# Performance work log

Measured on AMD Instinct MI355X. Metric: run time of the kernel, lower is better.

## Reference

```python
import jax, jax.numpy as jnp
import numpy as np

EPS = 1e-4

def setup_inputs() -> dict:
    key = jax.random.key(0)
    x = jax.random.normal(key, (16, 256, 8192), dtype=jnp.float32)
    return {"x": x}

def reference(x):
    # x: [B, C, T]; cumulative (causal) normalization along time axis
    T = x.shape[-1]
    count = jnp.arange(1, T + 1, dtype=x.dtype).reshape(1, 1, T)
    cum_sum = jnp.cumsum(x, axis=-1)
    cum_pow_sum = jnp.cumsum(x * x, axis=-1)
    cum_mean = cum_sum / count
    cum_var = cum_pow_sum / count - cum_mean * cum_mean
    cum_std = jnp.sqrt(cum_var + EPS)
    return (x - cum_mean) / cum_std
```

## Files before the change

### kernel.cpp

```cpp
#include <hip/hip_runtime.h>
#include <math.h>

#define ROW_T   8192
#define THREADS 256
#define ITEMS   32
#define EPSV    1e-4f

__device__ __forceinline__ int pad_idx(int i) { return i + (i >> 5); }

__global__ __launch_bounds__(THREADS, 4)
void cumnorm_kernel(const float* __restrict__ x, float* __restrict__ out) {
    __shared__ float lds[ROW_T + ROW_T / 32];
    __shared__ float wsum[4];
    __shared__ float wssum[4];

    const int t = threadIdx.x;
    const long long rowbase = (long long)blockIdx.x * ROW_T;
    const float* __restrict__ xr = x + rowbase;
    float* __restrict__ outr = out + rowbase;

    #pragma unroll
    for (int j = 0; j < 8; ++j) {
        const int fi = (j * THREADS + t) * 4;
        const float4 v = *reinterpret_cast<const float4*>(xr + fi);
        lds[pad_idx(fi + 0)] = v.x;
        lds[pad_idx(fi + 1)] = v.y;
        lds[pad_idx(fi + 2)] = v.z;
        lds[pad_idx(fi + 3)] = v.w;
    }
    __syncthreads();

    float xv[ITEMS];
    float s = 0.f, ss = 0.f;
    const int cbase = t * 33;
    #pragma unroll
    for (int j = 0; j < ITEMS; ++j) {
        const float v = lds[cbase + j];
        xv[j] = v;
        s += v;
        ss += v * v;
    }

    const int lane = t & 63;
    const int wid  = t >> 6;
    float is = s, iss = ss;
    #pragma unroll
    for (int off = 1; off < 64; off <<= 1) {
        const float us  = __shfl_up(is, off);
        const float uss = __shfl_up(iss, off);
        if (lane >= off) { is += us; iss += uss; }
    }
    if (lane == 63) { wsum[wid] = is; wssum[wid] = iss; }
    __syncthreads();

    float carry_s = 0.f, carry_ss = 0.f;
    #pragma unroll
    for (int w = 0; w < 4; ++w) {
        if (w < wid) { carry_s += wsum[w]; carry_ss += wssum[w]; }
    }
    float S  = carry_s  + (is  - s);
    float SS = carry_ss + (iss - ss);

    const int ebase = t * ITEMS;
    #pragma unroll
    for (int j = 0; j < ITEMS; ++j) {
        const float v = xv[j];
        S  += v;
        SS += v * v;
        const float inv  = 1.0f / (float)(ebase + j + 1);
        const float mean = S * inv;
        const float var  = fmaf(SS, inv, -(mean * mean));
        lds[cbase + j] = (v - mean) * rsqrtf(var + EPSV);
    }
    __syncthreads();

    #pragma unroll
    for (int j = 0; j < 8; ++j) {
        const int fi = (j * THREADS + t) * 4;
        float4 v;
        v.x = lds[pad_idx(fi + 0)];
        v.y = lds[pad_idx(fi + 1)];
        v.z = lds[pad_idx(fi + 2)];
        v.w = lds[pad_idx(fi + 3)];
        *reinterpret_cast<float4*>(outr + fi) = v;
    }
}

extern "C" void kernel_launch(void* const* d_in, const int* in_sizes, int n_in,
                              void* d_out, int out_size, void* d_ws, size_t ws_size,
                              hipStream_t stream) {
    const float* x = (const float*)d_in[0];
    float* out = (float*)d_out;
    const int rows = out_size / ROW_T;
    cumnorm_kernel<<<rows, THREADS, 0, stream>>>(x, out);
}
```

Baseline: 230.6 us.

## Halve LDS staging buffer, store outputs directly from registers, use fast rcp/rsq

Stages the row through LDS in two halves of 4096 elements, so LDS per block drops by half and the launch bound rises to 8 blocks per CU. The output transpose through LDS and its barrier are removed: each thread writes its 32 contiguous results straight to global memory as float4 stores. The intent is higher occupancy and less LDS traffic, at the cost of strided (non-coalesced across lanes) global stores. Exact division and rsqrtf are replaced with hardware rcp/rsq builtins, which are less precise.

New measurement: 246.7 us. 1.07x slower.

```diff
diff --git a/kernel.cpp b/kernel.cpp
--- a/kernel.cpp
+++ b/kernel.cpp
@@ -1,16 +1,17 @@
 #include <hip/hip_runtime.h>
-#include <math.h>
 
 #define ROW_T   8192
 #define THREADS 256
 #define ITEMS   32
+#define HALF    4096
 #define EPSV    1e-4f
 
-__device__ __forceinline__ int pad_idx(int i) { return i + (i >> 5); }
+__device__ __forceinline__ float fast_rcp(float v) { return __builtin_amdgcn_rcpf(v); }
+__device__ __forceinline__ float fast_rsq(float v) { return __builtin_amdgcn_rsqf(v); }
 
-__global__ __launch_bounds__(THREADS, 4)
+__global__ __launch_bounds__(THREADS, 8)
 void cumnorm_kernel(const float* __restrict__ x, float* __restrict__ out) {
-    __shared__ float lds[ROW_T + ROW_T / 32];
+    __shared__ float lds[HALF + HALF / 32];
     __shared__ float wsum[4];
     __shared__ float wssum[4];
 
@@ -19,26 +20,42 @@
     const float* __restrict__ xr = x + rowbase;
     float* __restrict__ outr = out + rowbase;
 
+    float xv[ITEMS];
+
     #pragma unroll
-    for (int j = 0; j < 8; ++j) {
+    for (int j = 0; j < 4; ++j) {
         const int fi = (j * THREADS + t) * 4;
         const float4 v = *reinterpret_cast<const float4*>(xr + fi);
-        lds[pad_idx(fi + 0)] = v.x;
-        lds[pad_idx(fi + 1)] = v.y;
-        lds[pad_idx(fi + 2)] = v.z;
-        lds[pad_idx(fi + 3)] = v.w;
+        const int p = fi + (fi >> 5);
+        lds[p + 0] = v.x; lds[p + 1] = v.y; lds[p + 2] = v.z; lds[p + 3] = v.w;
+    }
+    __syncthreads();
+    if (t < 128) {
+        const int cb = t * 33;
+        #pragma unroll
+        for (int j = 0; j < ITEMS; ++j) xv[j] = lds[cb + j];
     }
     __syncthreads();
 
-    float xv[ITEMS];
+    #pragma unroll
+    for (int j = 0; j < 4; ++j) {
+        const int fi = (j * THREADS + t) * 4;
+        const float4 v = *reinterpret_cast<const float4*>(xr + HALF + fi);
+        const int p = fi + (fi >> 5);
+        lds[p + 0] = v.x; lds[p + 1] = v.y; lds[p + 2] = v.z; lds[p + 3] = v.w;
+    }
+    __syncthreads();
+    if (t >= 128) {
+        const int cb = (t - 128) * 33;
+        #pragma unroll
+        for (int j = 0; j < ITEMS; ++j) xv[j] = lds[cb + j];
+    }
+
     float s = 0.f, ss = 0.f;
-    const int cbase = t * 33;
     #pragma unroll
     for (int j = 0; j < ITEMS; ++j) {
-        const float v = lds[cbase + j];
-        xv[j] = v;
-        s += v;
-        ss += v * v;
+        s += xv[j];
+        ss = fmaf(xv[j], xv[j], ss);
     }
 
     const int lane = t & 63;
@@ -65,24 +82,20 @@
     #pragma unroll
     for (int j = 0; j < ITEMS; ++j) {
         const float v = xv[j];
-        S  += v;
-        SS += v * v;
-        const float inv  = 1.0f / (float)(ebase + j + 1);
+        S += v;
+        SS = fmaf(v, v, SS);
+        const float inv  = fast_rcp((float)(ebase + j + 1));
         const float mean = S * inv;
         const float var  = fmaf(SS, inv, -(mean * mean));
-        lds[cbase + j] = (v - mean) * rsqrtf(var + EPSV);
+        xv[j] = (v - mean) * fast_rsq(var + EPSV);
     }
-    __syncthreads();
 
     #pragma unroll
     for (int j = 0; j < 8; ++j) {
-        const int fi = (j * THREADS + t) * 4;
         float4 v;
-        v.x = lds[pad_idx(fi + 0)];
-        v.y = lds[pad_idx(fi + 1)];
-        v.z = lds[pad_idx(fi + 2)];
-        v.w = lds[pad_idx(fi + 3)];
-        *reinterpret_cast<float4*>(outr + fi) = v;
+        v.x = xv[4 * j + 0]; v.y = xv[4 * j + 1];
+        v.z = xv[4 * j + 2]; v.w = xv[4 * j + 3];
+        *reinterpret_cast<float4*>(outr + ebase + j * 4) = v;
     }
 }
 
```

## Assign one row per wavefront with tiled register-prefetched scan and fast intrinsics

Applied to the files above, without the earlier changes.

Each wavefront now processes a whole row in four tiles of 2048 elements. The running sum and sum-of-squares are carried in registers across tiles, so the block-wide __syncthreads and cross-wave sums are no longer needed. The next tile's global loads are issued into registers before the current tile is computed, to overlap memory with compute. Division and rsqrt are replaced by the hardware rcp/rsq intrinsics. The cost is fewer blocks (1024 down to 256) and a serial dependence across tiles within each wave, which could expose memory latency.

Result: no change. 231.6 us (+0.5%).

```diff
diff --git a/kernel.cpp b/kernel.cpp
--- a/kernel.cpp
+++ b/kernel.cpp
@@ -1,88 +1,94 @@
 #include <hip/hip_runtime.h>
-#include <math.h>
 
 #define ROW_T   8192
-#define THREADS 256
-#define ITEMS   32
+#define TILE    2048
+#define NT      4
+#define WAVES   4
+#define THREADS (WAVES * 64)
+#define WSLOT   (TILE + TILE / 32)
 #define EPSV    1e-4f
-
-__device__ __forceinline__ int pad_idx(int i) { return i + (i >> 5); }
 
 __global__ __launch_bounds__(THREADS, 4)
 void cumnorm_kernel(const float* __restrict__ x, float* __restrict__ out) {
-    __shared__ float lds[ROW_T + ROW_T / 32];
-    __shared__ float wsum[4];
-    __shared__ float wssum[4];
+    __shared__ float lds[WAVES * WSLOT];
 
-    const int t = threadIdx.x;
-    const long long rowbase = (long long)blockIdx.x * ROW_T;
-    const float* __restrict__ xr = x + rowbase;
-    float* __restrict__ outr = out + rowbase;
+    const int t    = threadIdx.x;
+    const int lane = t & 63;
+    const int wid  = t >> 6;
+    float* __restrict__ sl = lds + wid * WSLOT;
+
+    const int row = blockIdx.x * WAVES + wid;
+    const float* __restrict__ xr   = x   + (long long)row * ROW_T;
+    float* __restrict__       outr = out + (long long)row * ROW_T;
+
+    float carry_s = 0.f, carry_ss = 0.f;
+
+    float4 pf[8];
+    #pragma unroll
+    for (int j = 0; j < 8; ++j)
+        pf[j] = *reinterpret_cast<const float4*>(xr + j * 256 + lane * 4);
 
     #pragma unroll
-    for (int j = 0; j < 8; ++j) {
-        const int fi = (j * THREADS + t) * 4;
-        const float4 v = *reinterpret_cast<const float4*>(xr + fi);
-        lds[pad_idx(fi + 0)] = v.x;
-        lds[pad_idx(fi + 1)] = v.y;
-        lds[pad_idx(fi + 2)] = v.z;
-        lds[pad_idx(fi + 3)] = v.w;
-    }
-    __syncthreads();
+    for (int tt = 0; tt < NT; ++tt) {
+        #pragma unroll
+        for (int j = 0; j < 8; ++j) {
+            const int e = j * 256 + lane * 4;
+            const int p = e + (e >> 5);
+            sl[p + 0] = pf[j].x; sl[p + 1] = pf[j].y;
+            sl[p + 2] = pf[j].z; sl[p + 3] = pf[j].w;
+        }
 
-    float xv[ITEMS];
-    float s = 0.f, ss = 0.f;
-    const int cbase = t * 33;
-    #pragma unroll
-    for (int j = 0; j < ITEMS; ++j) {
-        const float v = lds[cbase + j];
-        xv[j] = v;
-        s += v;
-        ss += v * v;
-    }
+        if (tt + 1 < NT) {
+            #pragma unroll
+            for (int j = 0; j < 8; ++j)
+                pf[j] = *reinterpret_cast<const float4*>(
+                    xr + (tt + 1) * TILE + j * 256 + lane * 4);
+        }
 
-    const int lane = t & 63;
-    const int wid  = t >> 6;
-    float is = s, iss = ss;
-    #pragma unroll
-    for (int off = 1; off < 64; off <<= 1) {
-        const float us  = __shfl_up(is, off);
-        const float uss = __shfl_up(iss, off);
-        if (lane >= off) { is += us; iss += uss; }
-    }
-    if (lane == 63) { wsum[wid] = is; wssum[wid] = iss; }
-    __syncthreads();
+        float xv[32];
+        const int cb = lane * 33;
+        float s = 0.f, ss = 0.f;
+        #pragma unroll
+        for (int j = 0; j < 32; ++j) {
+            const float v = sl[cb + j];
+            xv[j] = v;
+            s += v;
+            ss = fmaf(v, v, ss);
+        }
 
-    float carry_s = 0.f, carry_ss = 0.f;
-    #pragma unroll
-    for (int w = 0; w < 4; ++w) {
-        if (w < wid) { carry_s += wsum[w]; carry_ss += wssum[w]; }
-    }
-    float S  = carry_s  + (is  - s);
-    float SS = carry_ss + (iss - ss);
+        float is = s, iss = ss;
+        #pragma unroll
+        for (int off = 1; off < 64; off <<= 1) {
+            const float us  = __shfl_up(is, off);
+            const float uss = __shfl_up(iss, off);
+            if (lane >= off) { is += us; iss += uss; }
+        }
+        float S  = carry_s  + (is  - s);
+        float SS = carry_ss + (iss - ss);
+        carry_s  += __shfl(is, 63);
+        carry_ss += __shfl(iss, 63);
 
-    const int ebase = t * ITEMS;
-    #pragma unroll
-    for (int j = 0; j < ITEMS; ++j) {
-        const float v = xv[j];
-        S  += v;
-        SS += v * v;
-        const float inv  = 1.0f / (float)(ebase + j + 1);
-        const float mean = S * inv;
-        const float var  = fmaf(SS, inv, -(mean * mean));
-        lds[cbase + j] = (v - mean) * rsqrtf(var + EPSV);
-    }
-    __syncthreads();
+        const int ebase = tt * TILE + lane * 32;
+        #pragma unroll
+        for (int j = 0; j < 32; ++j) {
+            const float v = xv[j];
+            S += v;
+            SS = fmaf(v, v, SS);
+            const float inv  = __builtin_amdgcn_rcpf((float)(ebase + j + 1));
+            const float mean = S * inv;
+            const float var  = fmaf(SS, inv, -(mean * mean));
+            sl[cb + j] = (v - mean) * __builtin_amdgcn_rsqf(var + EPSV);
+        }
 
-    #pragma unroll
-    for (int j = 0; j < 8; ++j) {
-        const int fi = (j * THREADS + t) * 4;
-        float4 v;
-        v.x = lds[pad_idx(fi + 0)];
-        v.y = lds[pad_idx(fi + 1)];
-        v.z = lds[pad_idx(fi + 2)];
-        v.w = lds[pad_idx(fi + 3)];
-        *reinterpret_cast<float4*>(outr + fi) = v;
+        #pragma unroll
+        for (int j = 0; j < 8; ++j) {
+            const int e = j * 256 + lane * 4;
+            const int p = e + (e >> 5);
+            float4 v;
+            v.x = sl[p + 0]; v.y = sl[p + 1];
+            v.z = sl[p + 2]; v.w = sl[p + 3];
+            *reinterpret_cast<float4*>(outr + tt * TILE + e) = v;
+        }
     }
 }
 
@@ -92,5 +98,5 @@
     const float* x = (const float*)d_in[0];
     float* out = (float*)d_out;
     const int rows = out_size / ROW_T;
-    cumnorm_kernel<<<rows, THREADS, 0, stream>>>(x, out);
+    cumnorm_kernel<<<rows / WAVES, THREADS, 0, stream>>>(x, out);
 }
```

## Replace LDS-staged row scan with register-streamed tiled scan and prefetch

Applied to the files above, without the earlier changes.

The kernel no longer stages the whole 8192-element row in LDS. Each block now walks the row in 8 sequential tiles of 1024 elements, one float4 per thread. The next tile's global load is prefetched while the current one is scanned, and the running carry is kept in registers across tiles using a double-buffered cross-wave total. Dropping the 33 KB LDS buffer lets more blocks fit per CU, and fast rcp/rsq builtins replace the IEEE divide. The cost is one barrier per tile and a serial dependency chain across the tiles. The approximate reciprocal may also differ slightly in precision.

Result: no change. 228.7 us (-0.8%).

```diff
diff --git a/kernel.cpp b/kernel.cpp
--- a/kernel.cpp
+++ b/kernel.cpp
@@ -1,88 +1,92 @@
 #include <hip/hip_runtime.h>
-#include <math.h>
 
 #define ROW_T   8192
 #define THREADS 256
-#define ITEMS   32
+#define ITEMS   4
+#define STILE   (THREADS * ITEMS)
+#define NST     (ROW_T / STILE)
 #define EPSV    1e-4f
 
-__device__ __forceinline__ int pad_idx(int i) { return i + (i >> 5); }
+__global__ __launch_bounds__(THREADS, 8)
+void cumnorm_kernel(const float* __restrict__ x, float* __restrict__ out) {
+    __shared__ float wbs[2][4];
+    __shared__ float wbss[2][4];
 
-__global__ __launch_bounds__(THREADS, 4)
-void cumnorm_kernel(const float* __restrict__ x, float* __restrict__ out) {
-    __shared__ float lds[ROW_T + ROW_T / 32];
-    __shared__ float wsum[4];
-    __shared__ float wssum[4];
+    const int t    = threadIdx.x;
+    const int lane = t & 63;
+    const int wid  = t >> 6;
 
-    const int t = threadIdx.x;
-    const long long rowbase = (long long)blockIdx.x * ROW_T;
-    const float* __restrict__ xr = x + rowbase;
-    float* __restrict__ outr = out + rowbase;
+    const float* __restrict__ xr   = x   + (long long)blockIdx.x * ROW_T;
+    float* __restrict__       outr = out + (long long)blockIdx.x * ROW_T;
+
+    float carry_s = 0.f, carry_ss = 0.f;
+
+    float4 cur = *reinterpret_cast<const float4*>(xr + t * ITEMS);
+    float4 nxt;
 
     #pragma unroll
-    for (int j = 0; j < 8; ++j) {
-        const int fi = (j * THREADS + t) * 4;
-        const float4 v = *reinterpret_cast<const float4*>(xr + fi);
-        lds[pad_idx(fi + 0)] = v.x;
-        lds[pad_idx(fi + 1)] = v.y;
-        lds[pad_idx(fi + 2)] = v.z;
-        lds[pad_idx(fi + 3)] = v.w;
-    }
-    __syncthreads();
+    for (int k = 0; k < NST; ++k) {
+        if (k + 1 < NST)
+            nxt = *reinterpret_cast<const float4*>(xr + (k + 1) * STILE + t * ITEMS);
 
-    float xv[ITEMS];
-    float s = 0.f, ss = 0.f;
-    const int cbase = t * 33;
-    #pragma unroll
-    for (int j = 0; j < ITEMS; ++j) {
-        const float v = lds[cbase + j];
-        xv[j] = v;
-        s += v;
-        ss += v * v;
-    }
+        float s  = ((cur.x + cur.y) + (cur.z + cur.w));
+        float ss = fmaf(cur.x, cur.x, fmaf(cur.y, cur.y,
+                   fmaf(cur.z, cur.z, cur.w * cur.w)));
 
-    const int lane = t & 63;
-    const int wid  = t >> 6;
-    float is = s, iss = ss;
-    #pragma unroll
-    for (int off = 1; off < 64; off <<= 1) {
-        const float us  = __shfl_up(is, off);
-        const float uss = __shfl_up(iss, off);
-        if (lane >= off) { is += us; iss += uss; }
-    }
-    if (lane == 63) { wsum[wid] = is; wssum[wid] = iss; }
-    __syncthreads();
+        float is = s, iss = ss;
+        #pragma unroll
+        for (int off = 1; off < 64; off <<= 1) {
+            const float us  = __shfl_up(is, off);
+            const float uss = __shfl_up(iss, off);
+            if (lane >= off) { is += us; iss += uss; }
+        }
+        if (lane == 63) { wbs[k & 1][wid] = is; wbss[k & 1][wid] = iss; }
+        __syncthreads();
 
-    float carry_s = 0.f, carry_ss = 0.f;
-    #pragma unroll
-    for (int w = 0; w < 4; ++w) {
-        if (w < wid) { carry_s += wsum[w]; carry_ss += wssum[w]; }
-    }
-    float S  = carry_s  + (is  - s);
-    float SS = carry_ss + (iss - ss);
+        float cs = carry_s, css = carry_ss;
+        #pragma unroll
+        for (int w = 0; w < 4; ++w) {
+            const float a = wbs[k & 1][w], b = wbss[k & 1][w];
+            if (w < wid) { cs += a; css += b; }
+            carry_s += a; carry_ss += b;
+        }
 
-    const int ebase = t * ITEMS;
-    #pragma unroll
-    for (int j = 0; j < ITEMS; ++j) {
-        const float v = xv[j];
-        S  += v;
-        SS += v * v;
-        const float inv  = 1.0f / (float)(ebase + j + 1);
-        const float mean = S * inv;
-        const float var  = fmaf(SS, inv, -(mean * mean));
-        lds[cbase + j] = (v - mean) * rsqrtf(var + EPSV);
-    }
-    __syncthreads();
+        float S  = cs  + (is  - s);
+        float SS = css + (iss - ss);
 
-    #pragma unroll
-    for (int j = 0; j < 8; ++j) {
-        const int fi = (j * THREADS + t) * 4;
-        float4 v;
-        v.x = lds[pad_idx(fi + 0)];
-        v.y = lds[pad_idx(fi + 1)];
-        v.z = lds[pad_idx(fi + 2)];
-        v.w = lds[pad_idx(fi + 3)];
-        *reinterpret_cast<float4*>(outr + fi) = v;
+        const int e0 = k * STILE + t * ITEMS;
+        float4 o;
+        {
+            const float v = cur.x; S += v; SS = fmaf(v, v, SS);
+            const float inv = __builtin_amdgcn_rcpf((float)(e0 + 1));
+            const float mean = S * inv;
+            const float var  = fmaf(SS, inv, -(mean * mean));
+            o.x = (v - mean) * __builtin_amdgcn_rsqf(var + EPSV);
+        }
+        {
+            const float v = cur.y; S += v; SS = fmaf(v, v, SS);
+            const float inv = __builtin_amdgcn_rcpf((float)(e0 + 2));
+            const float mean = S * inv;
+            const float var  = fmaf(SS, inv, -(mean * mean));
+            o.y = (v - mean) * __builtin_amdgcn_rsqf(var + EPSV);
+        }
+        {
+            const float v = cur.z; S += v; SS = fmaf(v, v, SS);
+            const float inv = __builtin_amdgcn_rcpf((float)(e0 + 3));
+            const float mean = S * inv;
+            const float var  = fmaf(SS, inv, -(mean * mean));
+            o.z = (v - mean) * __builtin_amdgcn_rsqf(var + EPSV);
+        }
+        {
+            const float v = cur.w; S += v; SS = fmaf(v, v, SS);
+            const float inv = __builtin_amdgcn_rcpf((float)(e0 + 4));
+            const float mean = S * inv;
+            const float var  = fmaf(SS, inv, -(mean * mean));
+            o.w = (v - mean) * __builtin_amdgcn_rsqf(var + EPSV);
+        }
+
+        *reinterpret_cast<float4*>(outr + e0) = o;
+        cur = nxt;
     }
 }
 
```
